# Performance work log

Measured on AMD Instinct MI355X. Metric: run time of the kernel, lower is better.

Reference implementation:

```python
import jax, jax.numpy as jnp
import numpy as np

INF = 1e+24
DK = 16


def setup_inputs() -> dict:
    key = jax.random.key(0)
    ks = jax.random.split(key, 9)
    B, T, D = 64, 512, 1024
    x = jax.random.normal(ks[0], (B, T, D), dtype=jnp.float32)
    padding_mask = jax.random.randint(ks[1], (B, T, 1), 0, 2) > 0
    s = 1.0 / np.sqrt(D)
    Wq = jax.random.normal(ks[2], (D, DK), dtype=jnp.float32) * s
    bq = jnp.zeros((DK,), dtype=jnp.float32)
    Wk = jax.random.normal(ks[3], (D, DK), dtype=jnp.float32) * s
    bk = jnp.zeros((DK,), dtype=jnp.float32)
    Wv = jax.random.normal(ks[4], (D, D), dtype=jnp.float32) * s
    bv = jnp.zeros((D,), dtype=jnp.float32)
    return {"x": x, "padding_mask": padding_mask, "Wq": Wq, "bq": bq,
            "Wk": Wk, "bk": bk, "Wv": Wv, "bv": bv}


def reference(x, padding_mask, Wq, bq, Wk, bk, Wv, bv):
    # x: [B,T,D]; padding_mask: [B,T,1] bool
    q = x @ Wq + bq                      # [B,T,dk]
    k = x @ Wk + bk                      # [B,T,dk]
    v = x @ Wv + bv                      # [B,T,D]
    # original writes -INF into k at padded positions (broadcast over dk)
    k = jnp.where(padding_mask, jnp.float32(-INF), k)
    # NOTE: original multiplies by sqrt(dk) (misnamed _inv_dk)
    att = jnp.einsum('btd,bsd->bts', q, k) * jnp.sqrt(jnp.float32(DK))
    T = x.shape[1]
    causal = jnp.triu(jnp.ones((T, T), dtype=bool), k=1)  # [T,T]
    att = jnp.where(causal[None, :, :], jnp.float32(-INF), att)
    return jnp.einsum('bts,bsd->btd', jax.nn.softmax(att, axis=2), v)
```

## Files before the change

### kernel.cpp

```cpp
#include <hip/hip_runtime.h>
#include <hip/hip_bf16.h>
#include <stdint.h>

#define NEG_BIG (-1e24f)

typedef __attribute__((ext_vector_type(8))) short bf16x8;
typedef __attribute__((ext_vector_type(4))) float f32x4;

#define AS1 __attribute__((address_space(1)))
#define AS3 __attribute__((address_space(3)))

__device__ __forceinline__ void gload_lds16(const void* g, void* l) {
    __builtin_amdgcn_global_load_lds((AS1 unsigned*)g, (AS3 unsigned*)l, 16, 0, 0);
}

__device__ __forceinline__ unsigned short f2bf(float f) {
    union { float f; unsigned u; } v; v.f = f;
    return (unsigned short)((v.u + 0x7FFFu + ((v.u >> 16) & 1u)) >> 16);
}

__global__ void detect_mask_kernel(const unsigned* pm, int* flag) {
    __shared__ int notI, notF;
    if (threadIdx.x == 0) { notI = 0; notF = 0; }
    __syncthreads();
    int li = 0, lf = 0;
    for (int i = threadIdx.x; i < 8192; i += 256) {
        unsigned v = pm[i];
        if (v > 1u) li = 1;
        if (v != 0u && v != 0x3F800000u) lf = 1;
    }
    if (li) atomicOr(&notI, 1);
    if (lf) atomicOr(&notF, 1);
    __syncthreads();
    if (threadIdx.x == 0) *flag = notI ? (notF ? 1 : 2) : 0;
}

__global__ __launch_bounds__(256, 4)
void qk_conv_kernel(const float* __restrict__ x,
                    const float* __restrict__ Wq, const float* __restrict__ bq,
                    const float* __restrict__ Wk, const float* __restrict__ bk,
                    const void* __restrict__ pm, const int* __restrict__ pmflag,
                    unsigned short* __restrict__ xbf,
                    float* __restrict__ qo, float* __restrict__ ko) {
    __shared__ float xs[64 * 65];
    const int tid = threadIdx.x;
    const int r0 = blockIdx.x * 64;
    const int lane = tid & 63;
    const int wsel = __builtin_amdgcn_readfirstlane(tid >> 6);
    const int jb = (wsel & 1) * 8;
    const float* __restrict__ W = (wsel < 2) ? Wq : Wk;

    const int sr_base = tid >> 4;
    const int sd = (tid & 15) * 4;

    float acc[8];
#pragma unroll
    for (int j = 0; j < 8; j++) acc[j] = 0.f;

    for (int c0 = 0; c0 < 1024; c0 += 64) {
#pragma unroll
        for (int p = 0; p < 4; p++) {
            const int sr = sr_base + p * 16;
            const float4 xv = *(const float4*)(x + (size_t)(r0 + sr) * 1024 + c0 + sd);
            uint2 pk;
            pk.x = (unsigned)f2bf(xv.x) | ((unsigned)f2bf(xv.y) << 16);
            pk.y = (unsigned)f2bf(xv.z) | ((unsigned)f2bf(xv.w) << 16);
            *(uint2*)(xbf + (size_t)(r0 + sr) * 1024 + c0 + sd) = pk;
            xs[sr * 65 + sd + 0] = xv.x;
            xs[sr * 65 + sd + 1] = xv.y;
            xs[sr * 65 + sd + 2] = xv.z;
            xs[sr * 65 + sd + 3] = xv.w;
        }
        __syncthreads();
#pragma unroll 4
        for (int d = 0; d < 64; d++) {
            const int du = c0 + d;
            const float* __restrict__ w = W + (size_t)du * 16 + jb;
            const float xv = xs[lane * 65 + d];
#pragma unroll
            for (int j = 0; j < 8; j++) acc[j] = fmaf(xv, w[j], acc[j]);
        }
        __syncthreads();
    }

    const int grow = r0 + lane;
    if (wsel < 2) {
        float4 a, b2;
        a.x = acc[0] + bq[jb + 0]; a.y = acc[1] + bq[jb + 1];
        a.z = acc[2] + bq[jb + 2]; a.w = acc[3] + bq[jb + 3];
        b2.x = acc[4] + bq[jb + 4]; b2.y = acc[5] + bq[jb + 5];
        b2.z = acc[6] + bq[jb + 6]; b2.w = acc[7] + bq[jb + 7];
        *(float4*)(qo + (size_t)grow * 16 + jb) = a;
        *(float4*)(qo + (size_t)grow * 16 + jb + 4) = b2;
    } else {
        const int flag = *pmflag;
        bool mk;
        if (flag == 1) mk = ((const unsigned char*)pm)[grow] != 0;
        else           mk = ((const unsigned*)pm)[grow] != 0;
        float4 a, b2;
        if (mk) {
            a.x = a.y = a.z = a.w = NEG_BIG;
            b2 = a;
        } else {
            a.x = acc[0] + bk[jb + 0]; a.y = acc[1] + bk[jb + 1];
            a.z = acc[2] + bk[jb + 2]; a.w = acc[3] + bk[jb + 3];
            b2.x = acc[4] + bk[jb + 4]; b2.y = acc[5] + bk[jb + 5];
            b2.z = acc[6] + bk[jb + 6]; b2.w = acc[7] + bk[jb + 7];
        }
        *(float4*)(ko + (size_t)grow * 16 + jb) = a;
        *(float4*)(ko + (size_t)grow * 16 + jb + 4) = b2;
    }
}

__global__ void wvt_kernel(const float* __restrict__ Wv, unsigned short* __restrict__ WvT) {
    __shared__ float tile[32][33];
    const int k0 = blockIdx.x * 32, n0 = blockIdx.y * 32;
    const int tid = threadIdx.x;
#pragma unroll
    for (int i = 0; i < 4; i++) {
        int idx = i * 256 + tid;
        int r = idx >> 5, c = idx & 31;
        tile[r][c] = Wv[(size_t)(k0 + r) * 1024 + n0 + c];
    }
    __syncthreads();
#pragma unroll
    for (int i = 0; i < 4; i++) {
        int idx = i * 256 + tid;
        int r = idx >> 5, c = idx & 31;
        WvT[(size_t)(n0 + r) * 1024 + k0 + c] = f2bf(tile[c][r]);
    }
}

__global__ __launch_bounds__(256, 2)
void vgemm_kernel(const unsigned short* __restrict__ A,
                  const unsigned short* __restrict__ Bt,
                  const float* __restrict__ bias,
                  unsigned short* __restrict__ vTg) {
    __shared__ __align__(16) unsigned short smem[17408];
    unsigned short* As = smem;
    unsigned short* Bs = smem + 4096;
    const int bid = blockIdx.x;
    const int c = bid & 7;
    const int g = bid >> 3;
    const int mt = c * 32 + (g >> 3);
    const int nt = g & 7;
    const int m0 = mt * 128;
    const int n0 = nt * 128;
    const int tid = threadIdx.x;
    const int lane = tid & 63;
    const int wave = tid >> 6;
    const int wm = (wave & 1) * 64;
    const int wn = (wave >> 1) * 64;
    const int l15 = lane & 15;
    const int quad = lane >> 4;
    const int arow = tid >> 2;
    const int acol = (tid & 3) * 8;
    f32x4 acc[4][4];
#pragma unroll
    for (int i = 0; i < 4; i++)
#pragma unroll
        for (int j = 0; j < 4; j++)
#pragma unroll
            for (int r = 0; r < 4; r++) acc[i][j][r] = 0.f;

    for (int k0 = 0; k0 < 1024; k0 += 32) {
        gload_lds16(A + (size_t)(m0 + arow) * 1024 + k0 + acol, As + tid * 8);
        gload_lds16(A + (size_t)(m0 + 64 + arow) * 1024 + k0 + acol, As + 2048 + tid * 8);
        gload_lds16(Bt + (size_t)(n0 + arow) * 1024 + k0 + acol, Bs + tid * 8);
        gload_lds16(Bt + (size_t)(n0 + 64 + arow) * 1024 + k0 + acol, Bs + 2048 + tid * 8);
        __syncthreads();
        bf16x8 af[4], bfr[4];
#pragma unroll
        for (int i = 0; i < 4; i++) {
            af[i]  = *(const bf16x8*)(As + (wm + i * 16 + l15) * 32 + quad * 8);
            bfr[i] = *(const bf16x8*)(Bs + (wn + i * 16 + l15) * 32 + quad * 8);
        }
#pragma unroll
        for (int i = 0; i < 4; i++)
#pragma unroll
            for (int j = 0; j < 4; j++)
                acc[i][j] = __builtin_amdgcn_mfma_f32_16x16x32_bf16(af[i], bfr[j], acc[i][j], 0, 0, 0);
        __syncthreads();
    }
    unsigned short* vt = smem;
#pragma unroll
    for (int j = 0; j < 4; j++) {
        const int e_local = wn + j * 16 + l15;
        const float bb = bias[n0 + e_local];
#pragma unroll
        for (int i = 0; i < 4; i++) {
            const int s_base = wm + i * 16 + quad * 4;
            unsigned short h0 = f2bf(acc[i][j][0] + bb);
            unsigned short h1 = f2bf(acc[i][j][1] + bb);
            unsigned short h2 = f2bf(acc[i][j][2] + bb);
            unsigned short h3 = f2bf(acc[i][j][3] + bb);
            uint2 u;
            u.x = (unsigned)h0 | ((unsigned)h1 << 16);
            u.y = (unsigned)h2 | ((unsigned)h3 << 16);
            *(uint2*)(vt + e_local * 136 + s_base) = u;
        }
    }
    __syncthreads();
    const int b = m0 >> 9;
    const int sbase = m0 & 511;
#pragma unroll
    for (int p = 0; p < 8; p++) {
        const int idx = p * 256 + tid;
        const int e = idx >> 4;
        const int s8 = (idx & 15) * 8;
        uint4 val = *(const uint4*)(vt + e * 136 + s8);
        *(uint4*)(vTg + ((size_t)b * 1024 + n0 + e) * 512 + sbase + s8) = val;
    }
}

__global__ __launch_bounds__(256, 2)
void score_kernel(const float* __restrict__ q, const float* __restrict__ k,
                  unsigned short* __restrict__ P, float* __restrict__ isum) {
    __shared__ float Kt[512 * 16];
    __shared__ float Qt[128 * 16];
    __shared__ float redm[2][128];
    __shared__ float reds[2][128];
    __shared__ unsigned short Pt[2][64][132];
    const int tid = threadIdx.x;
    const int b = blockIdx.y;
    const int t0 = blockIdx.x * 128;
    {
        const float4* ks = (const float4*)(k + (size_t)b * 512 * 16);
        float4* kd = (float4*)Kt;
#pragma unroll
        for (int i = 0; i < 8; i++) kd[i * 256 + tid] = ks[i * 256 + tid];
        const float4* qs = (const float4*)(q + ((size_t)b * 512 + t0) * 16);
        float4* qd = (float4*)Qt;
#pragma unroll
        for (int i = 0; i < 2; i++) qd[i * 256 + tid] = qs[i * 256 + tid];
    }
    __syncthreads();
    const int row = tid & 127;
    const int half = tid >> 7;
    const int sbeg = half * 256;
    const int tglob = t0 + row;
    float qr[16];
#pragma unroll
    for (int j = 0; j < 16; j++) qr[j] = Qt[row * 16 + j];

    float m = -INFINITY;
    for (int s = sbeg; s < sbeg + 256; s++) {
        const float* kk = Kt + s * 16;
        float dot = 0.f;
#pragma unroll
        for (int j = 0; j < 16; j++) dot = fmaf(qr[j], kk[j], dot);
        float sc = (s > tglob) ? NEG_BIG : dot * 4.0f;
        m = fmaxf(m, sc);
    }
    redm[half][row] = m;
    __syncthreads();
    const float M = fmaxf(redm[0][row], redm[1][row]);
    float sum = 0.f;
    for (int ph = 0; ph < 4; ph++) {
        const int c0 = sbeg + ph * 64;
        for (int s = c0; s < c0 + 64; s++) {
            const float* kk = Kt + s * 16;
            float dot = 0.f;
#pragma unroll
            for (int j = 0; j < 16; j++) dot = fmaf(qr[j], kk[j], dot);
            float sc = (s > tglob) ? NEG_BIG : dot * 4.0f;
            float p = __expf(sc - M);
            sum += p;
            Pt[half][s - c0][row] = f2bf(p);
        }
        __syncthreads();
#pragma unroll
        for (int i = 0; i < 8; i++) {
            int li = i * 256 + tid;
            int h = li >> 10;
            int r = (li >> 3) & 127;
            int cg = li & 7;
            union { unsigned short u[8]; uint4 v; } tmp;
#pragma unroll
            for (int j = 0; j < 8; j++) tmp.u[j] = Pt[h][cg * 8 + j][r];
            *(uint4*)(P + ((size_t)(b * 512 + t0 + r)) * 512 + h * 256 + ph * 64 + cg * 8) = tmp.v;
        }
        __syncthreads();
    }
    reds[half][row] = sum;
    __syncthreads();
    if (half == 0) {
        float tot = reds[0][row] + reds[1][row];
        isum[(size_t)b * 512 + tglob] = 1.0f / tot;
    }
}

__global__ __launch_bounds__(256, 2)
void pv_kernel(const unsigned short* __restrict__ P,
               const unsigned short* __restrict__ vT,
               const float* __restrict__ isum,
               float* __restrict__ out) {
    __shared__ unsigned short As[128 * 32];
    __shared__ unsigned short Bs[128 * 32];
    const int bid = blockIdx.x;
    const int c = bid & 7;
    const int g = bid >> 3;
    const int b = c * 8 + (g >> 5);
    const int rem = g & 31;
    const int m0 = (rem >> 3) * 128;
    const int n0 = (rem & 7) * 128;
    const int tid = threadIdx.x;
    const int lane = tid & 63;
    const int wave = tid >> 6;
    const int wm = (wave & 1) * 64;
    const int wn = (wave >> 1) * 64;
    const int l15 = lane & 15;
    const int quad = lane >> 4;
    const int arow = tid >> 2;
    const int acol = (tid & 3) * 8;
    const unsigned short* Ab = P + (size_t)b * 512 * 512;
    const unsigned short* Bb = vT + (size_t)b * 1024 * 512;
    f32x4 acc[4][4];
#pragma unroll
    for (int i = 0; i < 4; i++)
#pragma unroll
        for (int j = 0; j < 4; j++)
#pragma unroll
            for (int r = 0; r < 4; r++) acc[i][j][r] = 0.f;

    for (int k0 = 0; k0 < 512; k0 += 32) {
        gload_lds16(Ab + (size_t)(m0 + arow) * 512 + k0 + acol, As + tid * 8);
        gload_lds16(Ab + (size_t)(m0 + 64 + arow) * 512 + k0 + acol, As + 2048 + tid * 8);
        gload_lds16(Bb + (size_t)(n0 + arow) * 512 + k0 + acol, Bs + tid * 8);
        gload_lds16(Bb + (size_t)(n0 + 64 + arow) * 512 + k0 + acol, Bs + 2048 + tid * 8);
        __syncthreads();
        bf16x8 af[4], bfr[4];
#pragma unroll
        for (int i = 0; i < 4; i++) {
            af[i]  = *(const bf16x8*)(As + (wm + i * 16 + l15) * 32 + quad * 8);
            bfr[i] = *(const bf16x8*)(Bs + (wn + i * 16 + l15) * 32 + quad * 8);
        }
#pragma unroll
        for (int i = 0; i < 4; i++)
#pragma unroll
            for (int j = 0; j < 4; j++)
                acc[i][j] = __builtin_amdgcn_mfma_f32_16x16x32_bf16(af[i], bfr[j], acc[i][j], 0, 0, 0);
        __syncthreads();
    }
#pragma unroll
    for (int i = 0; i < 4; i++) {
#pragma unroll
        for (int r = 0; r < 4; r++) {
            const int trow = m0 + wm + i * 16 + quad * 4 + r;
            const float sc = isum[(size_t)b * 512 + trow];
#pragma unroll
            for (int j = 0; j < 4; j++) {
                const int ncol = n0 + wn + j * 16 + l15;
                out[((size_t)b * 512 + trow) * 1024 + ncol] = acc[i][j][r] * sc;
            }
        }
    }
}

extern "C" void kernel_launch(void* const* d_in, const int* in_sizes, int n_in,
                              void* d_out, int out_size, void* d_ws, size_t ws_size,
                              hipStream_t stream) {
    const float* x  = (const float*)d_in[0];
    const void*  pm = d_in[1];
    const float* Wq = (const float*)d_in[2];
    const float* bq = (const float*)d_in[3];
    const float* Wk = (const float*)d_in[4];
    const float* bk = (const float*)d_in[5];
    const float* Wv = (const float*)d_in[6];
    const float* bv = (const float*)d_in[7];
    float* out = (float*)d_out;

    char* ws = (char*)d_ws;
    const size_t MB = 1024 * 1024;
    unsigned short* xbf = (unsigned short*)ws;
    unsigned short* Pun = (unsigned short*)ws;
    unsigned short* vT  = (unsigned short*)(ws + 64 * MB);
    float* qbuf = (float*)(ws + 128 * MB);
    float* kbuf = (float*)(ws + 130 * MB);
    unsigned short* WvT = (unsigned short*)(ws + 132 * MB);
    float* isum = (float*)(ws + 134 * MB);
    int* flag   = (int*)(ws + 135 * MB);

    detect_mask_kernel<<<1, 256, 0, stream>>>((const unsigned*)pm, flag);
    qk_conv_kernel<<<512, 256, 0, stream>>>(x, Wq, bq, Wk, bk, pm, flag, xbf, qbuf, kbuf);
    wvt_kernel<<<dim3(32, 32), 256, 0, stream>>>(Wv, WvT);
    vgemm_kernel<<<2048, 256, 0, stream>>>(xbf, WvT, bv, vT);
    score_kernel<<<dim3(4, 64), 256, 0, stream>>>(qbuf, kbuf, Pun, isum);
    pv_kernel<<<2048, 256, 0, stream>>>(Pun, vT, isum, out);
}
```

Baseline: 550.1 us.

## Split-K the Q/K projection across four wave slices with a register-prefetched x tile

The Q/K projection kernel grows from 256 to 1024 threads per block. Each group of four waves now handles a 16-column slice of every 64-wide K chunk, and the partial sums are combined through an LDS reduction before the bias and padding mask are applied. The next x tile is prefetched into registers while the current chunk is being computed, which overlaps the global load with the FMA loop. This is meant to cut the long serial dependent FMA chain per wave and expose more memory parallelism. In exchange it adds an extra reduction pass and barrier, and the aggressive launch bounds could force register pressure or spills.

```diff
diff --git a/kernel.cpp b/kernel.cpp
--- a/kernel.cpp
+++ b/kernel.cpp
@@ -35,81 +35,89 @@
     if (threadIdx.x == 0) *flag = notI ? (notF ? 1 : 2) : 0;
 }
 
-__global__ __launch_bounds__(256, 4)
+__global__ __launch_bounds__(1024, 8)
 void qk_conv_kernel(const float* __restrict__ x,
                     const float* __restrict__ Wq, const float* __restrict__ bq,
                     const float* __restrict__ Wk, const float* __restrict__ bk,
                     const void* __restrict__ pm, const int* __restrict__ pmflag,
                     unsigned short* __restrict__ xbf,
                     float* __restrict__ qo, float* __restrict__ ko) {
-    __shared__ float xs[64 * 65];
+    __shared__ float smem[4 * 64 * 33];
+    float* xs = smem;
     const int tid = threadIdx.x;
     const int r0 = blockIdx.x * 64;
     const int lane = tid & 63;
-    const int wsel = __builtin_amdgcn_readfirstlane(tid >> 6);
-    const int jb = (wsel & 1) * 8;
-    const float* __restrict__ W = (wsel < 2) ? Wq : Wk;
-
-    const int sr_base = tid >> 4;
+    const int wv = __builtin_amdgcn_readfirstlane(tid >> 6);
+    const int g = wv & 3;
+    const int sl = wv >> 2;
+    const int jb = (g & 1) * 8;
+    const int d0 = sl * 16;
+    const float* __restrict__ W = (g < 2) ? Wq : Wk;
+
+    const int sr = tid >> 4;
     const int sd = (tid & 15) * 4;
+    const float* __restrict__ xp = x + (size_t)(r0 + sr) * 1024 + sd;
+    unsigned short* __restrict__ xbp = xbf + (size_t)(r0 + sr) * 1024 + sd;
 
     float acc[8];
 #pragma unroll
     for (int j = 0; j < 8; j++) acc[j] = 0.f;
 
+    float4 xv = *(const float4*)xp;
     for (int c0 = 0; c0 < 1024; c0 += 64) {
-#pragma unroll
-        for (int p = 0; p < 4; p++) {
-            const int sr = sr_base + p * 16;
-            const float4 xv = *(const float4*)(x + (size_t)(r0 + sr) * 1024 + c0 + sd);
-            uint2 pk;
-            pk.x = (unsigned)f2bf(xv.x) | ((unsigned)f2bf(xv.y) << 16);
-            pk.y = (unsigned)f2bf(xv.z) | ((unsigned)f2bf(xv.w) << 16);
-            *(uint2*)(xbf + (size_t)(r0 + sr) * 1024 + c0 + sd) = pk;
-            xs[sr * 65 + sd + 0] = xv.x;
-            xs[sr * 65 + sd + 1] = xv.y;
-            xs[sr * 65 + sd + 2] = xv.z;
-            xs[sr * 65 + sd + 3] = xv.w;
-        }
-        __syncthreads();
+        uint2 pk;
+        pk.x = (unsigned)f2bf(xv.x) | ((unsigned)f2bf(xv.y) << 16);
+        pk.y = (unsigned)f2bf(xv.z) | ((unsigned)f2bf(xv.w) << 16);
+        *(uint2*)(xbp + c0) = pk;
+        xs[sr * 65 + sd + 0] = xv.x;
+        xs[sr * 65 + sd + 1] = xv.y;
+        xs[sr * 65 + sd + 2] = xv.z;
+        xs[sr * 65 + sd + 3] = xv.w;
+        __syncthreads();
+        if (c0 + 64 < 1024) xv = *(const float4*)(xp + c0 + 64);
+        const float* __restrict__ wrow = W + (size_t)(c0 + d0) * 16 + jb;
+        const float* __restrict__ xrow = xs + lane * 65 + d0;
 #pragma unroll 4
-        for (int d = 0; d < 64; d++) {
-            const int du = c0 + d;
-            const float* __restrict__ w = W + (size_t)du * 16 + jb;
-            const float xv = xs[lane * 65 + d];
-#pragma unroll
-            for (int j = 0; j < 8; j++) acc[j] = fmaf(xv, w[j], acc[j]);
-        }
-        __syncthreads();
-    }
-
-    const int grow = r0 + lane;
-    if (wsel < 2) {
-        float4 a, b2;
-        a.x = acc[0] + bq[jb + 0]; a.y = acc[1] + bq[jb + 1];
-        a.z = acc[2] + bq[jb + 2]; a.w = acc[3] + bq[jb + 3];
-        b2.x = acc[4] + bq[jb + 4]; b2.y = acc[5] + bq[jb + 5];
-        b2.z = acc[6] + bq[jb + 6]; b2.w = acc[7] + bq[jb + 7];
-        *(float4*)(qo + (size_t)grow * 16 + jb) = a;
-        *(float4*)(qo + (size_t)grow * 16 + jb + 4) = b2;
+        for (int dd = 0; dd < 16; dd++) {
+            const float xvv = xrow[dd];
+            const float* __restrict__ w = wrow + (size_t)dd * 16;
+#pragma unroll
+            for (int j = 0; j < 8; j++) acc[j] = fmaf(xvv, w[j], acc[j]);
+        }
+        __syncthreads();
+    }
+
+    float* red = smem;
+    const int cb = jb + (g >> 1) * 16;
+    {
+        float* rr = red + ((size_t)(sl * 64 + lane)) * 33 + cb;
+#pragma unroll
+        for (int j = 0; j < 8; j++) rr[j] = acc[j];
+    }
+    __syncthreads();
+
+    const int row = tid >> 4;
+    const int c = tid & 15;
+    const int grow = r0 + row;
+    const float qv = red[(size_t)row * 33 + c]
+                   + red[(size_t)(64 + row) * 33 + c]
+                   + red[(size_t)(128 + row) * 33 + c]
+                   + red[(size_t)(192 + row) * 33 + c] + bq[c];
+    qo[(size_t)grow * 16 + c] = qv;
+    const int flag = *pmflag;
+    bool mk;
+    if (flag == 1) mk = ((const unsigned char*)pm)[grow] != 0;
+    else           mk = ((const unsigned*)pm)[grow] != 0;
+    float kv;
+    if (mk) {
+        kv = NEG_BIG;
     } else {
-        const int flag = *pmflag;
-        bool mk;
-        if (flag == 1) mk = ((const unsigned char*)pm)[grow] != 0;
-        else           mk = ((const unsigned*)pm)[grow] != 0;
-        float4 a, b2;
-        if (mk) {
-            a.x = a.y = a.z = a.w = NEG_BIG;
-            b2 = a;
-        } else {
-            a.x = acc[0] + bk[jb + 0]; a.y = acc[1] + bk[jb + 1];
-            a.z = acc[2] + bk[jb + 2]; a.w = acc[3] + bk[jb + 3];
-            b2.x = acc[4] + bk[jb + 4]; b2.y = acc[5] + bk[jb + 5];
-            b2.z = acc[6] + bk[jb + 6]; b2.w = acc[7] + bk[jb + 7];
-        }
-        *(float4*)(ko + (size_t)grow * 16 + jb) = a;
-        *(float4*)(ko + (size_t)grow * 16 + jb + 4) = b2;
-    }
+        kv = red[(size_t)row * 33 + 16 + c]
+           + red[(size_t)(64 + row) * 33 + 16 + c]
+           + red[(size_t)(128 + row) * 33 + 16 + c]
+           + red[(size_t)(192 + row) * 33 + 16 + c] + bk[c];
+    }
+    ko[(size_t)grow * 16 + c] = kv;
 }
 
 __global__ void wvt_kernel(const float* __restrict__ Wv, unsigned short* __restrict__ WvT) {
@@ -382,7 +390,7 @@
     int* flag   = (int*)(ws + 135 * MB);
 
     detect_mask_kernel<<<1, 256, 0, stream>>>((const unsigned*)pm, flag);
-    qk_conv_kernel<<<512, 256, 0, stream>>>(x, Wq, bq, Wk, bk, pm, flag, xbf, qbuf, kbuf);
+    qk_conv_kernel<<<512, 1024, 0, stream>>>(x, Wq, bq, Wk, bk, pm, flag, xbf, qbuf, kbuf);
     wvt_kernel<<<dim3(32, 32), 256, 0, stream>>>(Wv, WvT);
     vgemm_kernel<<<2048, 256, 0, stream>>>(xbf, WvT, bv, vT);
     score_kernel<<<dim3(4, 64), 256, 0, stream>>>(qbuf, kbuf, Pun, isum);
```

Measured after the change: 472.2 us. -14.2%, faster.
